# Kernel optimization log

Measured on AMD Instinct MI355X. Metric: run time of the kernel, lower is better.

Reference implementation:

```python
import jax, jax.numpy as jnp
import numpy as np


def setup_inputs() -> dict:
    key = jax.random.key(0)
    kx, kw = jax.random.split(key)
    x = jax.random.normal(kx, (32, 256, 56, 56), dtype=jnp.float32)
    weight = jax.random.uniform(kw, (256, 256, 3, 3), dtype=jnp.float32) * 0.001
    return {"x": x, "weight": weight}


def reference(x, weight):
    # --- binarize activations with straight-through estimator ---
    # forward value = sign(x); gradient flows through clamp(x, -1, 1)
    clipped_x = jnp.clip(x, -1.0, 1.0)
    bx = jax.lax.stop_gradient(jnp.sign(x) - clipped_x) + clipped_x

    # --- binarize weights (per-output-channel mean-centered, scaled sign) ---
    w = weight
    # subtract per-output-channel mean over (in_c, kh, kw)
    bw = w - jnp.mean(w.reshape(w.shape[0], -1), axis=-1)[:, None, None, None]
    # per-output-channel scaling factor = mean |bw| (detached)
    scale = jnp.mean(jnp.abs(bw), axis=(1, 2, 3), keepdims=True)
    scale = jax.lax.stop_gradient(scale)
    clipped_w = jnp.clip(bw, -1.0, 1.0)
    binary_w = jax.lax.stop_gradient(scale * jnp.sign(bw) - clipped_w) + clipped_w

    # --- conv2d, NCHW / OIHW, stride 1, padding 1 ---
    y = jax.lax.conv_general_dilated(
        bx, binary_w,
        window_strides=(1, 1),
        padding=((1, 1), (1, 1)),
        dimension_numbers=("NCHW", "OIHW", "NCHW"),
    )
    return y
```

## Files before the change

kernel.cpp:

```cpp
#include <hip/hip_runtime.h>
#include <cstdint>
#include <cstddef>

#define N_ 32
#define C_ 256
#define H_ 56
#define W_ 56

typedef int v4i __attribute__((ext_vector_type(4)));

static constexpr size_t WB_BYTES = 36ull * 16 * 64 * 16;
static constexpr size_t SC_OFF   = WB_BYTES;

__device__ __forceinline__ uint32_t sgnw(uint32_t u) {
    return (u & 0x7fffffffu) ? (((uint32_t)(((int)u) >> 31) | 1u) & 0xffu) : 0u;
}
__device__ __forceinline__ uint32_t sgnb(uint32_t u) {
    return ((uint32_t)(((int)u) >> 31) | 1u) & 0xffu;
}
__device__ __forceinline__ uint32_t pack4f(float4 v) {
    return sgnb(__float_as_uint(v.x)) | (sgnb(__float_as_uint(v.y)) << 8) |
           (sgnb(__float_as_uint(v.z)) << 16) | (sgnb(__float_as_uint(v.w)) << 24);
}

__global__ __launch_bounds__(256) void pack_w(const float* __restrict__ wt,
                                              char* __restrict__ wB,
                                              float* __restrict__ scaleg) {
    __shared__ double red[256];
    int o = blockIdx.x, tid = threadIdx.x;
    const float* wo = wt + (size_t)o * 2304;

    double s = 0;
    for (int j = tid; j < 2304; j += 256) s += (double)wo[j];
    red[tid] = s;
    __syncthreads();
    for (int k = 128; k > 0; k >>= 1) {
        if (tid < k) red[tid] += red[tid + k];
        __syncthreads();
    }
    double mean = red[0] / 2304.0;
    __syncthreads();

    double s2 = 0;
    for (int j = tid; j < 2304; j += 256) s2 += fabs((double)wo[j] - mean);
    red[tid] = s2;
    __syncthreads();
    for (int k = 128; k > 0; k >>= 1) {
        if (tid < k) red[tid] += red[tid + k];
        __syncthreads();
    }
    if (tid == 0) scaleg[o] = (float)(red[0] / 2304.0);

    if (tid < 144) {
        int kiter = tid >> 2, q = tid & 3;
        int tap = kiter >> 2, cb = kiter & 3;
        int kh = tap / 3, kw = tap - kh * 3;
        int words[4];
        for (int g = 0; g < 4; ++g) {
            int word = 0;
            for (int b = 0; b < 4; ++b) {
                int c = cb * 64 + q * 16 + g * 4 + b;
                double v = (double)wo[c * 9 + kh * 3 + kw];
                int sg = (v > mean) - (v < mean);
                word |= (sg & 0xff) << (8 * b);
            }
            words[g] = word;
        }
        v4i pk = {words[0], words[1], words[2], words[3]};
        *(v4i*)(wB + (((size_t)kiter * 16 + (o >> 4)) * 64 + q * 16 + (o & 15)) * 16) = pk;
    }
}

__global__ __launch_bounds__(256, 2) void conv_mfma(const float* __restrict__ x,
                                                    const v4i* __restrict__ wB,
                                                    const float* __restrict__ scaleg,
                                                    float* __restrict__ out) {
    __shared__ char xs[4 * 58 * 256];
    int tid = threadIdx.x;
    int wave = tid >> 6, lane = tid & 63;

    int lin = blockIdx.x + 28 * blockIdx.y;
    int swz = (lin & 7) * 112 + (lin >> 3);
    int hp = swz % 28, n = swz / 28;
    int h0 = hp * 2;

    if (tid < 128) {
        int r  = tid >> 5;
        int c2 = tid & 31;
        int wp = (c2 >> 4) * 57;
        int ch = c2 & 15;
        int slot = (ch + wp) & 15;
        v4i z = {0, 0, 0, 0};
        *(v4i*)(xs + ((size_t)(r * 58 + wp) << 8) + (slot << 4)) = z;
    }

    auto unit = [&](int u) {
        int R   = u / 224;
        int rem = u - R * 224;
        int ch  = rem / 14;
        int wq  = rem - ch * 14;
        int ir  = h0 + R - 1;
        if (ir < 0 || ir > 55) {
            v4i z = {0, 0, 0, 0};
#pragma unroll
            for (int h = 0; h < 4; ++h) {
                int wp = 1 + wq * 4 + h;
                int slot = (ch + wp) & 15;
                *(v4i*)(xs + ((size_t)(R * 58 + wp) << 8) + (slot << 4)) = z;
            }
            return;
        }
        const float* xb = x + ((size_t)n * C_ + ch * 16) * 3136 + ir * 56 + wq * 4;
        uint32_t sw[16];
#pragma unroll
        for (int c = 0; c < 16; ++c)
            sw[c] = pack4f(*(const float4*)(xb + (size_t)c * 3136));
        uint32_t t[4][4];
#pragma unroll
        for (int p = 0; p < 4; ++p) {
            uint32_t lo01 = __builtin_amdgcn_perm(sw[4*p+1], sw[4*p+0], 0x05010400u);
            uint32_t hi01 = __builtin_amdgcn_perm(sw[4*p+1], sw[4*p+0], 0x07030602u);
            uint32_t lo23 = __builtin_amdgcn_perm(sw[4*p+3], sw[4*p+2], 0x05010400u);
            uint32_t hi23 = __builtin_amdgcn_perm(sw[4*p+3], sw[4*p+2], 0x07030602u);
            t[p][0] = __builtin_amdgcn_perm(lo23, lo01, 0x05040100u);
            t[p][1] = __builtin_amdgcn_perm(lo23, lo01, 0x07060302u);
            t[p][2] = __builtin_amdgcn_perm(hi23, hi01, 0x05040100u);
            t[p][3] = __builtin_amdgcn_perm(hi23, hi01, 0x07060302u);
        }
#pragma unroll
        for (int h = 0; h < 4; ++h) {
            int wp = 1 + wq * 4 + h;
            int slot = (ch + wp) & 15;
            v4i c4 = {(int)t[0][h], (int)t[1][h], (int)t[2][h], (int)t[3][h]};
            *(v4i*)(xs + ((size_t)(R * 58 + wp) << 8) + (slot << 4)) = c4;
        }
    };
    unit(tid);
    unit(tid + 256);
    unit(tid + 512);
    if (tid < 128) unit(tid + 768);

    int lm = lane & 15, q = lane >> 4;
    int og = wave;
    int kstart = __builtin_amdgcn_readfirstlane(wave * 9);

    int posb[7], slotb[7];
#pragma unroll
    for (int mf = 0; mf < 7; ++mf) {
        int m = mf * 16 + lm;
        int r = m / 56;
        int wof = m - r * 56;
        posb[mf]  = r * 58 + wof;
        slotb[mf] = q + wof;
    }

    v4i acc[7][4];
#pragma unroll
    for (int mf = 0; mf < 7; ++mf)
#pragma unroll
        for (int of = 0; of < 4; ++of) { v4i z = {0, 0, 0, 0}; acc[mf][of] = z; }

    const v4i* wBw = wB + (size_t)(og * 4) * 64 + lane;

    auto wrap = [&](int t) {
        int k = kstart + t;
        if (k >= 36) k -= 36;
        if (k >= 36) k -= 36;
        return k;
    };
    auto loadB = [&](int k, v4i (&b)[4]) {
#pragma unroll
        for (int of = 0; of < 4; ++of) b[of] = wBw[(size_t)k * 1024 + of * 64];
    };

    __syncthreads();

    v4i bR0[4], bR1[4], bR2[4];
    loadB(wrap(0), bR0);
    loadB(wrap(1), bR1);
    loadB(wrap(2), bR2);

    auto step = [&](v4i (&bReg)[4], int t) {
        int k = wrap(t);
        int tap = k >> 2, cb = k & 3;
        int dh = (tap * 11) >> 5;
        int dw = tap - dh * 3;
        int pofs = dh * 58 + dw;
        int sofs = cb * 4 + dw;
        v4i a[7];
#pragma unroll
        for (int mf = 0; mf < 7; ++mf) {
            int pos  = posb[mf] + pofs;
            int slot = (slotb[mf] + sofs) & 15;
            a[mf] = *(const v4i*)(xs + ((size_t)pos << 8) + ((size_t)slot << 4));
        }
        __builtin_amdgcn_s_setprio(1);
#pragma unroll
        for (int mf = 0; mf < 7; ++mf)
#pragma unroll
            for (int of = 0; of < 4; ++of)
                acc[mf][of] = __builtin_amdgcn_mfma_i32_16x16x64_i8(
                    a[mf], bReg[of], acc[mf][of], 0, 0, 0);
        __builtin_amdgcn_s_setprio(0);
        loadB(wrap(t + 3), bReg);
    };

    for (int t3 = 0; t3 < 12; ++t3) {
        int t = t3 * 3;
        step(bR0, t);
        step(bR1, t + 1);
        step(bR2, t + 2);
    }

#pragma unroll
    for (int of = 0; of < 4; ++of) {
        int o = (og * 4 + of) * 16 + lm;
        float s = scaleg[o];
#pragma unroll
        for (int mf = 0; mf < 7; ++mf) {
            int m  = mf * 16 + q * 4;
            int r  = m / 56;
            int wb = m - r * 56;
            float* ob = out + ((size_t)(n * C_ + o) * H_ + h0 + r) * W_ + wb;
            float4 v = {s * (float)acc[mf][of].x, s * (float)acc[mf][of].y,
                        s * (float)acc[mf][of].z, s * (float)acc[mf][of].w};
            *(float4*)ob = v;
        }
    }
}

extern "C" void kernel_launch(void* const* d_in, const int* in_sizes, int n_in,
                              void* d_out, int out_size, void* d_ws, size_t ws_size,
                              hipStream_t stream) {
    const float* x   = (const float*)d_in[0];
    const float* wgt = (const float*)d_in[1];
    float* out = (float*)d_out;
    char* ws = (char*)d_ws;

    char*  wb = ws;
    float* sg = (float*)(ws + SC_OFF);

    pack_w<<<dim3(256), dim3(256), 0, stream>>>(wgt, wb, sg);
    conv_mfma<<<dim3(28, N_), dim3(256), 0, stream>>>(x, (const v4i*)wb, sg, out);
}
```

Before: 244.7 us.

## Process two row-pairs per block with a rotating 4-row LDS ring buffer

Each block now computes four output rows in two passes instead of two rows. Input rows are held in a 4-slot circular LDS buffer, so the second pass only loads two new rows and reuses the two overlapping halo rows. This removes half of the redundant halo loads and binarize/pack work per output row. In exchange the grid is halved to 448 blocks, which lowers parallelism, and the extra barriers serialize the reload between the two compute passes.

```diff
diff --git a/kernel.cpp b/kernel.cpp
--- a/kernel.cpp
+++ b/kernel.cpp
@@ -79,34 +79,25 @@
     int tid = threadIdx.x;
     int wave = tid >> 6, lane = tid & 63;
 
-    int lin = blockIdx.x + 28 * blockIdx.y;
-    int swz = (lin & 7) * 112 + (lin >> 3);
-    int hp = swz % 28, n = swz / 28;
-    int h0 = hp * 2;
-
-    if (tid < 128) {
-        int r  = tid >> 5;
-        int c2 = tid & 31;
-        int wp = (c2 >> 4) * 57;
-        int ch = c2 & 15;
-        int slot = (ch + wp) & 15;
-        v4i z = {0, 0, 0, 0};
-        *(v4i*)(xs + ((size_t)(r * 58 + wp) << 8) + (slot << 4)) = z;
-    }
-
-    auto unit = [&](int u) {
+    int lin = blockIdx.x + 14 * blockIdx.y;
+    int swz = (lin & 7) * 56 + (lin >> 3);
+    int hq = swz % 14, n = swz / 14;
+    int h0a = hq * 4;
+
+    auto unit = [&](int ir0, int u) {
         int R   = u / 224;
         int rem = u - R * 224;
         int ch  = rem / 14;
         int wq  = rem - ch * 14;
-        int ir  = h0 + R - 1;
+        int ir  = ir0 + R;
+        int slot = ir & 3;
         if (ir < 0 || ir > 55) {
             v4i z = {0, 0, 0, 0};
 #pragma unroll
             for (int h = 0; h < 4; ++h) {
                 int wp = 1 + wq * 4 + h;
-                int slot = (ch + wp) & 15;
-                *(v4i*)(xs + ((size_t)(R * 58 + wp) << 8) + (slot << 4)) = z;
+                int s16 = (ch + wp) & 15;
+                *(v4i*)(xs + ((size_t)(slot * 58 + wp) << 8) + (s16 << 4)) = z;
             }
             return;
         }
@@ -130,35 +121,41 @@
 #pragma unroll
         for (int h = 0; h < 4; ++h) {
             int wp = 1 + wq * 4 + h;
-            int slot = (ch + wp) & 15;
+            int s16 = (ch + wp) & 15;
             v4i c4 = {(int)t[0][h], (int)t[1][h], (int)t[2][h], (int)t[3][h]};
-            *(v4i*)(xs + ((size_t)(R * 58 + wp) << 8) + (slot << 4)) = c4;
-        }
-    };
-    unit(tid);
-    unit(tid + 256);
-    unit(tid + 512);
-    if (tid < 128) unit(tid + 768);
+            *(v4i*)(xs + ((size_t)(slot * 58 + wp) << 8) + (s16 << 4)) = c4;
+        }
+    };
+    auto halo = [&](int ir0, int u) {
+        int r  = u >> 5;
+        int c2 = u & 31;
+        int slot = (ir0 + r) & 3;
+        int wp = (c2 >> 4) * 57;
+        int ch = c2 & 15;
+        int s16 = (ch + wp) & 15;
+        v4i z = {0, 0, 0, 0};
+        *(v4i*)(xs + ((size_t)(slot * 58 + wp) << 8) + (s16 << 4)) = z;
+    };
+
+    if (tid < 128) halo(h0a - 1, tid);
+    unit(h0a - 1, tid);
+    unit(h0a - 1, tid + 256);
+    unit(h0a - 1, tid + 512);
+    if (tid < 128) unit(h0a - 1, tid + 768);
 
     int lm = lane & 15, q = lane >> 4;
     int og = wave;
     int kstart = __builtin_amdgcn_readfirstlane(wave * 9);
 
-    int posb[7], slotb[7];
+    int wof[7], ro[7], slotb[7];
 #pragma unroll
     for (int mf = 0; mf < 7; ++mf) {
         int m = mf * 16 + lm;
         int r = m / 56;
-        int wof = m - r * 56;
-        posb[mf]  = r * 58 + wof;
-        slotb[mf] = q + wof;
-    }
-
-    v4i acc[7][4];
-#pragma unroll
-    for (int mf = 0; mf < 7; ++mf)
-#pragma unroll
-        for (int of = 0; of < 4; ++of) { v4i z = {0, 0, 0, 0}; acc[mf][of] = z; }
+        ro[mf]    = r;
+        wof[mf]   = m - r * 56;
+        slotb[mf] = q + wof[mf];
+    }
 
     const v4i* wBw = wB + (size_t)(og * 4) * 64 + lane;
 
@@ -173,60 +170,80 @@
         for (int of = 0; of < 4; ++of) b[of] = wBw[(size_t)k * 1024 + of * 64];
     };
 
-    __syncthreads();
-
-    v4i bR0[4], bR1[4], bR2[4];
-    loadB(wrap(0), bR0);
-    loadB(wrap(1), bR1);
-    loadB(wrap(2), bR2);
-
-    auto step = [&](v4i (&bReg)[4], int t) {
-        int k = wrap(t);
-        int tap = k >> 2, cb = k & 3;
-        int dh = (tap * 11) >> 5;
-        int dw = tap - dh * 3;
-        int pofs = dh * 58 + dw;
-        int sofs = cb * 4 + dw;
-        v4i a[7];
-#pragma unroll
-        for (int mf = 0; mf < 7; ++mf) {
-            int pos  = posb[mf] + pofs;
-            int slot = (slotb[mf] + sofs) & 15;
-            a[mf] = *(const v4i*)(xs + ((size_t)pos << 8) + ((size_t)slot << 4));
-        }
-        __builtin_amdgcn_s_setprio(1);
+    auto run_iter = [&](int h0it) {
+        v4i acc[7][4];
 #pragma unroll
         for (int mf = 0; mf < 7; ++mf)
 #pragma unroll
-            for (int of = 0; of < 4; ++of)
-                acc[mf][of] = __builtin_amdgcn_mfma_i32_16x16x64_i8(
-                    a[mf], bReg[of], acc[mf][of], 0, 0, 0);
-        __builtin_amdgcn_s_setprio(0);
-        loadB(wrap(t + 3), bReg);
-    };
-
-    for (int t3 = 0; t3 < 12; ++t3) {
-        int t = t3 * 3;
-        step(bR0, t);
-        step(bR1, t + 1);
-        step(bR2, t + 2);
-    }
-
-#pragma unroll
-    for (int of = 0; of < 4; ++of) {
-        int o = (og * 4 + of) * 16 + lm;
-        float s = scaleg[o];
-#pragma unroll
-        for (int mf = 0; mf < 7; ++mf) {
-            int m  = mf * 16 + q * 4;
-            int r  = m / 56;
-            int wb = m - r * 56;
-            float* ob = out + ((size_t)(n * C_ + o) * H_ + h0 + r) * W_ + wb;
-            float4 v = {s * (float)acc[mf][of].x, s * (float)acc[mf][of].y,
-                        s * (float)acc[mf][of].z, s * (float)acc[mf][of].w};
-            *(float4*)ob = v;
-        }
-    }
+            for (int of = 0; of < 4; ++of) { v4i z = {0, 0, 0, 0}; acc[mf][of] = z; }
+
+        v4i bR0[4], bR1[4], bR2[4];
+        loadB(wrap(0), bR0);
+        loadB(wrap(1), bR1);
+        loadB(wrap(2), bR2);
+
+        auto step = [&](v4i (&bReg)[4], int t) {
+            int k = wrap(t);
+            int tap = k >> 2, cb = k & 3;
+            int dh = (tap * 11) >> 5;
+            int dw = tap - dh * 3;
+            int s0 = (h0it - 1 + dh) & 3;
+            int s1 = (s0 + 1) & 3;
+            int p0 = s0 * 58 + dw;
+            int dpr = (s1 - s0) * 58;
+            int sofs = cb * 4 + dw;
+            v4i a[7];
+#pragma unroll
+            for (int mf = 0; mf < 7; ++mf) {
+                int pos = p0 + ro[mf] * dpr + wof[mf];
+                int s16 = (slotb[mf] + sofs) & 15;
+                a[mf] = *(const v4i*)(xs + ((size_t)pos << 8) + (s16 << 4));
+            }
+            __builtin_amdgcn_s_setprio(1);
+#pragma unroll
+            for (int mf = 0; mf < 7; ++mf)
+#pragma unroll
+                for (int of = 0; of < 4; ++of)
+                    acc[mf][of] = __builtin_amdgcn_mfma_i32_16x16x64_i8(
+                        a[mf], bReg[of], acc[mf][of], 0, 0, 0);
+            __builtin_amdgcn_s_setprio(0);
+            loadB(wrap(t + 3), bReg);
+        };
+
+        for (int t3 = 0; t3 < 12; ++t3) {
+            int t = t3 * 3;
+            step(bR0, t);
+            step(bR1, t + 1);
+            step(bR2, t + 2);
+        }
+
+#pragma unroll
+        for (int of = 0; of < 4; ++of) {
+            int o = (og * 4 + of) * 16 + lm;
+            float s = scaleg[o];
+#pragma unroll
+            for (int mf = 0; mf < 7; ++mf) {
+                int m  = mf * 16 + q * 4;
+                int r  = m / 56;
+                int wb = m - r * 56;
+                float* ob = out + ((size_t)(n * C_ + o) * H_ + h0it + r) * W_ + wb;
+                float4 v = {s * (float)acc[mf][of].x, s * (float)acc[mf][of].y,
+                            s * (float)acc[mf][of].z, s * (float)acc[mf][of].w};
+                *(float4*)ob = v;
+            }
+        }
+    };
+
+    __syncthreads();
+    run_iter(h0a);
+
+    __syncthreads();
+    if (tid < 64) halo(h0a + 3, tid);
+    unit(h0a + 3, tid);
+    if (tid < 192) unit(h0a + 3, tid + 256);
+    __syncthreads();
+
+    run_iter(h0a + 2);
 }
 
 extern "C" void kernel_launch(void* const* d_in, const int* in_sizes, int n_in,
@@ -241,5 +258,5 @@
     float* sg = (float*)(ws + SC_OFF);
 
     pack_w<<<dim3(256), dim3(256), 0, stream>>>(wgt, wb, sg);
-    conv_mfma<<<dim3(28, N_), dim3(256), 0, stream>>>(x, (const v4i*)wb, sg, out);
-}
+    conv_mfma<<<dim3(14, N_), dim3(256), 0, stream>>>(x, (const v4i*)wb, sg, out);
+}
```

Result: faster. 239.7 us (median of 2 runs) (-2.0%).
